# Kernel tuning notes

Measured on AMD Instinct MI355X. Metric: run time of the kernel, lower is better.

Reference implementation:

```python
import jax, jax.numpy as jnp
import numpy as np

N, E, C, H, EDGE_DIM, HID = 50000, 800000, 128, 8, 64, 512
D = C // H  # head dim = out_channels_conv


def layer_norm(x, g, b, eps=1e-5):
    mu = x.mean(-1, keepdims=True)
    var = ((x - mu) ** 2).mean(-1, keepdims=True)
    return (x - mu) * jax.lax.rsqrt(var + eps) * g + b


def _lin_init(k, fan_in, fan_out):
    s = 1.0 / np.sqrt(fan_in)
    kw, kb = jax.random.split(k)
    w = jax.random.uniform(kw, (fan_in, fan_out), minval=-s, maxval=s, dtype=jnp.float32)
    b = jax.random.uniform(kb, (fan_out,), minval=-s, maxval=s, dtype=jnp.float32)
    return w, b


def setup_inputs() -> dict:
    key = jax.random.key(0)
    ks = jax.random.split(key, 16)
    wq, bq = _lin_init(ks[0], C, C)
    wk, bk = _lin_init(ks[1], C, C)
    wv, bv = _lin_init(ks[2], C, C)
    ws, bs = _lin_init(ks[3], C, C)          # lin_self
    we, be = _lin_init(ks[4], EDGE_DIM, C)   # lin_edge
    wp, bp = _lin_init(ks[5], C, C)          # projection
    w1, b1 = _lin_init(ks[6], C, HID)        # node_dst_mlp[0]
    w2, b2 = _lin_init(ks[7], HID, C)        # node_dst_mlp[2]
    x = jax.random.normal(ks[8], (N, C), dtype=jnp.float32)
    edge_attr = jax.random.normal(ks[9], (E, EDGE_DIM), dtype=jnp.float32)
    edge_index = jax.random.randint(ks[10], (2, E), 0, N, dtype=jnp.int64)
    return dict(
        x=x, edge_attr=edge_attr, edge_index=edge_index,
        wq=wq, bq=bq, wk=wk, bk=bk, wv=wv, bv=bv, ws=ws, bs=bs,
        we=we, be=be, wp=wp, bp=bp, w1=w1, b1=b1, w2=w2, b2=b2,
        ln1_g=jnp.ones((C,), jnp.float32), ln1_b=jnp.zeros((C,), jnp.float32),
        ln2_g=jnp.ones((C,), jnp.float32), ln2_b=jnp.zeros((C,), jnp.float32),
    )


def reference(x, edge_attr, edge_index,
              wq, bq, wk, bk, wv, bv, ws, bs, we, be, wp, bp,
              w1, b1, w2, b2, ln1_g, ln1_b, ln2_g, ln2_b):
    src, dst = edge_index[0], edge_index[1]

    x_skip = x
    xn = layer_norm(x, ln1_g, ln1_b)                       # layer_norm_attention
    x_r = xn @ ws + bs                                     # lin_self residual
    q = (xn @ wq + bq).reshape(N, H, D)
    k = (xn @ wk + bk).reshape(N, H, D)
    v = (xn @ wv + bv).reshape(N, H, D)
    e = (edge_attr @ we + be).reshape(E, H, D)             # lin_edge (edge_pre_mlp = Identity)

    # edge-indexed multi-head attention: softmax over incoming edges per dst node
    ke = k[src] + e                                        # [E,H,D]
    alpha = jnp.einsum('ehd,ehd->eh', q[dst], ke) / np.sqrt(D)   # [E,H]
    amax = jax.lax.stop_gradient(jax.ops.segment_max(alpha, dst, num_segments=N))
    ex = jnp.exp(alpha - amax[dst])
    den = jax.ops.segment_sum(ex, dst, num_segments=N)
    w = ex / (den[dst] + 1e-16)                            # [E,H]
    out = jax.ops.segment_sum(w[:, :, None] * (v[src] + e), dst, num_segments=N)  # [N,H,D]
    out = out.reshape(N, C)

    out = (out + x_r) @ wp + bp                            # projection
    out = out + x_skip
    h = layer_norm(out, ln2_g, ln2_b)                      # layer_norm_mlp_dst
    h = jax.nn.gelu(h @ w1 + b1) @ w2 + b2                 # node_dst_mlp
    nodes_new = out + h
    return nodes_new, edge_attr
```

## Files before the change

kernel.cpp:

```cpp
#include <hip/hip_runtime.h>
#include <hip/hip_bf16.h>
#include <cstdio>

#define NN 50000
#define NE 800000
#define CC 128
#define EDIM 64
#define HIDN 512

using bf16 = __hip_bfloat16;
typedef short sh8 __attribute__((ext_vector_type(8)));
typedef float f32x4 __attribute__((ext_vector_type(4)));

static __device__ __forceinline__ float b2f(bf16 v){ return __bfloat162float(v); }
static __device__ __forceinline__ bf16 f2b(float v){ return __float2bfloat16(v); }
static __device__ __forceinline__ float u2f(unsigned short u){
    union { unsigned int i; float f; } w; w.i = ((unsigned int)u) << 16; return w.f;
}
static __device__ __forceinline__ unsigned short f2u(float f){
    bf16 b = __float2bfloat16(f);
    return *reinterpret_cast<unsigned short*>(&b);
}
static __device__ __forceinline__ float2 loadbf2(const bf16* p){
    __hip_bfloat162 v = *reinterpret_cast<const __hip_bfloat162*>(p);
    return make_float2(__bfloat162float(v.x), __bfloat162float(v.y));
}
static __device__ __forceinline__ float gelu_tanh(float x){
    const float c = 0.7978845608028654f;
    float u = c * (x + 0.044715f * x * x * x);
    return x / (1.0f + __expf(-2.0f * u));
}

constexpr size_t AL(size_t x){ return (x + 255) & ~(size_t)255; }
constexpr size_t OFF_FLAG = 0;
constexpr size_t OFF_DEG  = 256;
constexpr size_t OFF_ROW  = AL(OFF_DEG + (size_t)(NN + 1) * 4);
constexpr size_t OFF_CUR  = AL(OFF_ROW + (size_t)(NN + 1) * 4);
constexpr size_t OFF_EPOS = AL(OFF_CUR + (size_t)NN * 4);
constexpr size_t OFF_SRC  = AL(OFF_EPOS + (size_t)NE * 4);
constexpr size_t OFF_DST  = AL(OFF_SRC + (size_t)NE * 4);
constexpr size_t OFF_QC   = AL(OFF_DST + (size_t)NE * 4);
constexpr size_t OFF_KC   = AL(OFF_QC  + (size_t)NN * CC * 2);
constexpr size_t OFF_VC   = AL(OFF_KC  + (size_t)NN * CC * 2);
constexpr size_t OFF_ATT  = AL(OFF_VC  + (size_t)NN * CC * 2);
constexpr size_t OFF_PRM  = AL(OFF_ATT + (size_t)NN * CC * 2);
constexpr size_t PRM_ELEMS = 4*(16384+128) + 8192+128 + 16384+128 + 65536+512 + 65536+128 + 4*128;
constexpr size_t OFF_ALP  = AL(OFF_PRM + PRM_ELEMS * 2);
constexpr size_t OFF_VP   = AL(OFF_ALP + (size_t)NE * 8 * 4);
constexpr size_t OFF_XRC  = AL(OFF_VP + (size_t)NE * CC * 2);
constexpr size_t OFF_WFQ  = AL(OFF_XRC + (size_t)NN * CC * 2);
constexpr size_t OFF_WFK  = OFF_WFQ + 32768;
constexpr size_t OFF_WFV  = OFF_WFK + 32768;
constexpr size_t OFF_WFS  = OFF_WFV + 32768;
constexpr size_t OFF_WFP  = OFF_WFS + 32768;
constexpr size_t OFF_WF1  = OFF_WFP + 32768;
constexpr size_t OFF_WF2  = OFF_WF1 + 131072;
constexpr size_t OFF_WFE  = OFF_WF2 + 131072;
constexpr size_t OFF_BSUM = OFF_WFE + 16384;
constexpr size_t WS_NEED  = OFF_BSUM + 256;

__global__ void k_detect(const unsigned short* xw, const unsigned int* ew, int* flags){
    __shared__ int sw, sz;
    if (threadIdx.x == 0){ sw = 0; sz = 0; }
    __syncthreads();
    int w = 0;
    for (int i = threadIdx.x; i < 8192; i += 256){
        unsigned e = (xw[i] >> 7) & 0xFF;
        if (e == 0xFF || (e != 0 && (e < 0x60 || e > 0x90))) w++;
    }
    atomicAdd(&sw, w);
    int z = 0;
    for (int i = threadIdx.x; i < 2048; i += 256)
        if (ew[2*i+1] == 0u) z++;
    atomicAdd(&sz, z);
    __syncthreads();
    if (threadIdx.x == 0){
        flags[0] = (sw > 2048) ? 1 : 0;
        flags[1] = (sz > 1536) ? 1 : 0;
    }
}

struct CvtJob { const void* s; bf16* d; int n; };
struct CvtJobs { CvtJob j[20]; };
__global__ void k_cvt_all(CvtJobs jobs, const int* flags){
    const int f = flags[0];
    const int e = blockIdx.x >> 5;
    const CvtJob J = jobs.j[e];
    const int stride = 32 * 256;
    for (int i = (blockIdx.x & 31) * 256 + threadIdx.x; i < J.n; i += stride){
        if (f) J.d[i] = f2b(((const float*)J.s)[i]);
        else   J.d[i] = ((const bf16*)J.s)[i];
    }
}

__global__ void k_cvt_idx(const int* e32, int* srcI, int* dstI, int* deg, const int* flags){
    const int f = flags[1];
    int i = blockIdx.x * blockDim.x + threadIdx.x;
    const int stride = gridDim.x * blockDim.x;
    if (f){
        const long long* e64 = (const long long*)e32;
        for (; i < NE; i += stride){
            srcI[i] = (int)e64[i];
            const int d = (int)e64[NE + i];
            dstI[i] = d;
            atomicAdd(&deg[d], 1);
        }
    } else {
        for (; i < NE; i += stride){
            srcI[i] = e32[i];
            const int d = e32[NE + i];
            dstI[i] = d;
            atomicAdd(&deg[d], 1);
        }
    }
}

struct WJob { const bf16* W; bf16* WF; int K; int N; };
struct WJobs { WJob j[8]; };
__global__ void k_wprep_all(WJobs jobs){
    const WJob J = jobs.j[blockIdx.x / 48];
    const int KS = J.K >> 5;
    const int total = J.K * J.N;
    for (int o = (blockIdx.x % 48) * 256 + threadIdx.x; o < total; o += 48 * 256){
        const int j  = o & 7;
        const int ln = (o >> 3) & 63;
        const int tt = o >> 9;
        const int ks = tt % KS, ct = tt / KS;
        const int kk = (ks << 5) + ((ln >> 4) << 3) + j;
        const int c  = (ct << 4) + (ln & 15);
        J.WF[o] = J.W[kk * J.N + c];
    }
}

#define ASWZ(row, chunk)  (((row) << 8)  + ((((chunk) ^ ((row) & 15))) << 4))
#define HSWZ(row, chunk)  (((row) << 10) + ((((chunk) ^ ((row) & 15))) << 4))
#define EASWZ(row, chunk) (((row) << 7)  + ((((chunk) ^ ((row) & 7)))  << 4))

static __device__ __forceinline__ void gemm_nodes_128(
    const unsigned short* Abase, int row0, int lane,
    const bf16* __restrict__ WF, const bf16* __restrict__ bias,
    bf16* __restrict__ outp, int n0)
{
    const int rA = row0 + (lane & 15);
    sh8 af[4];
    #pragma unroll
    for (int ks = 0; ks < 4; ++ks)
        af[ks] = *(const sh8*)((const char*)Abase + ASWZ(rA, (ks << 2) + (lane >> 4)));
    f32x4 acc[8] = {};
    #pragma unroll
    for (int ks = 0; ks < 4; ++ks)
        #pragma unroll
        for (int ct = 0; ct < 8; ++ct){
            sh8 bfr = *(const sh8*)(WF + ((size_t)((ct << 2) + ks) * 64 + lane) * 8);
            acc[ct] = __builtin_amdgcn_mfma_f32_16x16x32_bf16(af[ks], bfr, acc[ct], 0, 0, 0);
        }
    #pragma unroll
    for (int ct = 0; ct < 8; ++ct){
        const int c = (ct << 4) + (lane & 15);
        const float bv = b2f(bias[c]);
        #pragma unroll
        for (int i = 0; i < 4; ++i){
            const int r = row0 + ((lane >> 4) << 2) + i;
            if (n0 + r < NN)
                outp[(size_t)(n0 + r) * CC + c] = f2b(acc[ct][i] + bv);
        }
    }
}

__global__ __launch_bounds__(256) void k_node_pre2(
    const void* __restrict__ x_raw, const int* __restrict__ flags,
    const bf16* __restrict__ WFq, const bf16* __restrict__ bq,
    const bf16* __restrict__ WFk, const bf16* __restrict__ bk,
    const bf16* __restrict__ WFv, const bf16* __restrict__ bv,
    const bf16* __restrict__ WFs, const bf16* __restrict__ bs,
    const bf16* __restrict__ g,  const bf16* __restrict__ bb,
    bf16* __restrict__ q, bf16* __restrict__ k, bf16* __restrict__ v,
    bf16* __restrict__ xr)
{
    __shared__ unsigned short A[64 * 128];
    const int t = threadIdx.x, lane = t & 63, wid = t >> 6;
    const int n0 = blockIdx.x * 64;

    if (flags[0]){
        const float* x = (const float*)x_raw;
        #pragma unroll
        for (int it = 0; it < 8; ++it){
            const int u = t + 256 * it;
            const int row = u >> 5, c = (u & 31) << 2;
            float4 a = make_float4(0.f, 0.f, 0.f, 0.f);
            if (n0 + row < NN)
                a = *(const float4*)&x[(size_t)(n0 + row) * CC + c];
            ushort4 b;
            b.x = f2u(a.x); b.y = f2u(a.y); b.z = f2u(a.z); b.w = f2u(a.w);
            *(ushort4*)((char*)A + ASWZ(row, c >> 3) + ((c & 7) << 1)) = b;
        }
    } else {
        const bf16* x = (const bf16*)x_raw;
        #pragma unroll
        for (int it = 0; it < 4; ++it){
            const int c8 = t + 256 * it;
            const int row = c8 >> 4, chunk = c8 & 15, col = chunk << 3;
            uint4 val = make_uint4(0u, 0u, 0u, 0u);
            if (n0 + row < NN)
                val = *(const uint4*)&x[(size_t)(n0 + row) * CC + col];
            *(uint4*)((char*)A + ASWZ(row, chunk)) = val;
        }
    }
    __syncthreads();

    {
        const int nd = wid * 16 + (lane & 15), qd = lane >> 4;
        float vals[32];
        #pragma unroll
        for (int i = 0; i < 4; ++i){
            uint4 u = *(const uint4*)((const char*)A + ASWZ(nd, (qd << 2) + i));
            unsigned uu[4] = {u.x, u.y, u.z, u.w};
            #pragma unroll
            for (int j2 = 0; j2 < 4; ++j2){
                vals[i*8 + j2*2]     = u2f((unsigned short)(uu[j2] & 0xFFFF));
                vals[i*8 + j2*2 + 1] = u2f((unsigned short)(uu[j2] >> 16));
            }
        }
        float s = 0.f;
        #pragma unroll
        for (int i = 0; i < 32; ++i) s += vals[i];
        s += __shfl_xor(s, 16); s += __shfl_xor(s, 32);
        const float mu = s * (1.0f / CC);
        float vv = 0.f;
        #pragma unroll
        for (int i = 0; i < 32; ++i){ const float d = vals[i] - mu; vv += d * d; }
        vv += __shfl_xor(vv, 16); vv += __shfl_xor(vv, 32);
        const float rstd = rsqrtf(vv * (1.0f / CC) + 1e-5f);
        #pragma unroll
        for (int i = 0; i < 4; ++i){
            unsigned w[4];
            #pragma unroll
            for (int j2 = 0; j2 < 4; ++j2){
                const int c0 = qd * 32 + i * 8 + j2 * 2;
                const float a0 = (vals[i*8+j2*2]   - mu) * rstd * b2f(g[c0])   + b2f(bb[c0]);
                const float a1 = (vals[i*8+j2*2+1] - mu) * rstd * b2f(g[c0+1]) + b2f(bb[c0+1]);
                w[j2] = (unsigned)f2u(a0) | ((unsigned)f2u(a1) << 16);
            }
            *(uint4*)((char*)A + ASWZ(nd, (qd << 2) + i)) = make_uint4(w[0], w[1], w[2], w[3]);
        }
    }
    __syncthreads();

    const int row0 = wid * 16;
    gemm_nodes_128(A, row0, lane, WFq, bq, q,  n0);
    gemm_nodes_128(A, row0, lane, WFk, bk, k,  n0);
    gemm_nodes_128(A, row0, lane, WFv, bv, v,  n0);
    gemm_nodes_128(A, row0, lane, WFs, bs, xr, n0);
}

__global__ __launch_bounds__(1024) void k_scan1(const int* __restrict__ deg,
                                                int* __restrict__ row, int* __restrict__ bsum){
    __shared__ int sb[1024];
    const int t = threadIdx.x;
    const int idx = blockIdx.x * 1024 + t;
    sb[t] = (idx < NN) ? deg[idx] : 0;
    __syncthreads();
    for (int off = 1; off < 1024; off <<= 1){
        int tv = (t >= off) ? sb[t - off] : 0;
        __syncthreads();
        sb[t] += tv;
        __syncthreads();
    }
    if (idx < NN) row[idx + 1] = sb[t];
    if (t == 1023) bsum[blockIdx.x] = sb[1023];
}

__global__ void k_scan2(int* __restrict__ bsum, int nb){
    int v = (threadIdx.x < nb) ? bsum[threadIdx.x] : 0;
    for (int off = 1; off < 64; off <<= 1){
        int u = __shfl_up(v, off);
        if (threadIdx.x >= off) v += u;
    }
    if (threadIdx.x < nb) bsum[threadIdx.x] = v;
}

__global__ __launch_bounds__(1024) void k_scan3(const int* __restrict__ bsum, int* __restrict__ row){
    const int idx = blockIdx.x * 1024 + threadIdx.x;
    const int add = (blockIdx.x > 0) ? bsum[blockIdx.x - 1] : 0;
    if (idx < NN) row[idx + 1] += add;
    if (idx == 0) row[0] = 0;
}

__global__ void k_scatter(const int* __restrict__ dst, const int* __restrict__ rowstart,
                          int* __restrict__ cursor, int* __restrict__ epos){
    const int i = blockIdx.x * blockDim.x + threadIdx.x;
    if (i < NE) {
        const int d = dst[i];
        const int p = atomicAdd(&cursor[d], 1);
        epos[i] = rowstart[d] + p;
    }
}

__global__ __launch_bounds__(256) void k_edge3(
    const void* __restrict__ ea_raw, const int* __restrict__ flags,
    const bf16* __restrict__ WFe, const bf16* __restrict__ be,
    const bf16* __restrict__ kv_q, const bf16* __restrict__ kv_k, const bf16* __restrict__ kv_v,
    const int* __restrict__ srcI, const int* __restrict__ dstI, const int* __restrict__ epos,
    float* __restrict__ alphap, unsigned short* __restrict__ vperm)
{
    __shared__ unsigned short EA[64 * 64];
    __shared__ unsigned short ET[64 * 128];
    const int t = threadIdx.x, lane = t & 63, wid = t >> 6;
    const int e0 = blockIdx.x * 64;

    if (flags[0]){
        const float* ea = (const float*)ea_raw;
        #pragma unroll
        for (int it = 0; it < 4; ++it){
            const int u = t + 256 * it;
            const int row = u >> 4, c = (u & 15) << 2;
            const float4 a = *(const float4*)&ea[(size_t)(e0 + row) * EDIM + c];
            ushort4 b;
            b.x = f2u(a.x); b.y = f2u(a.y); b.z = f2u(a.z); b.w = f2u(a.w);
            *(ushort4*)((char*)EA + EASWZ(row, c >> 3) + ((c & 7) << 1)) = b;
        }
    } else {
        const unsigned short* ea = (const unsigned short*)ea_raw;
        #pragma unroll
        for (int it = 0; it < 2; ++it){
            const int u = t + 256 * it;
            const int row = u >> 3, c = (u & 7) << 3;
            ushort4 lo = *(const ushort4*)&ea[(size_t)(e0 + row) * EDIM + c];
            ushort4 hi = *(const ushort4*)&ea[(size_t)(e0 + row) * EDIM + c + 4];
            *(ushort4*)((char*)EA + EASWZ(row, c >> 3)) = lo;
            *(ushort4*)((char*)EA + EASWZ(row, c >> 3) + 8) = hi;
        }
    }
    __syncthreads();

    const int row0 = wid * 16;
    {
        const int rA = row0 + (lane & 15);
        sh8 af[2];
        #pragma unroll
        for (int ks = 0; ks < 2; ++ks)
            af[ks] = *(const sh8*)((const char*)EA + EASWZ(rA, (ks << 2) + (lane >> 4)));
        f32x4 acc[8] = {};
        #pragma unroll
        for (int ks = 0; ks < 2; ++ks)
            #pragma unroll
            for (int ct = 0; ct < 8; ++ct){
                sh8 bfr = *(const sh8*)(WFe + ((size_t)((ct << 1) + ks) * 64 + lane) * 8);
                acc[ct] = __builtin_amdgcn_mfma_f32_16x16x32_bf16(af[ks], bfr, acc[ct], 0, 0, 0);
            }
        #pragma unroll
        for (int ct = 0; ct < 8; ++ct){
            const int c = (ct << 4) + (lane & 15);
            const float bv = b2f(be[c]);
            #pragma unroll
            for (int i = 0; i < 4; ++i){
                const int r = row0 + ((lane >> 4) << 2) + i;
                *(unsigned short*)((char*)ET + ASWZ(r, c >> 3) + ((c & 7) << 1)) =
                    f2u(acc[ct][i] + bv);
            }
        }
    }
    __syncthreads();

    const int g = t >> 5, cT = t & 31, c = cT << 2;
    #pragma unroll
    for (int i = 0; i < 8; ++i){
        const int eid = e0 + g * 8 + i;
        const int s = srcI[eid];
        const int d = dstI[eid];
        const int p = epos[eid];
        const ushort4 ev = *(const ushort4*)((const char*)ET + ASWZ(g * 8 + i, c >> 3) + ((c & 7) << 1));
        const ushort4 kr = *(const ushort4*)&kv_k[(size_t)s * CC + c];
        const ushort4 vr = *(const ushort4*)&kv_v[(size_t)s * CC + c];
        const ushort4 qr = *(const ushort4*)&kv_q[(size_t)d * CC + c];
        const float e0_ = u2f(ev.x), e1_ = u2f(ev.y), e2_ = u2f(ev.z), e3_ = u2f(ev.w);
        float part = u2f(qr.x) * (e0_ + u2f(kr.x)) + u2f(qr.y) * (e1_ + u2f(kr.y))
                   + u2f(qr.z) * (e2_ + u2f(kr.z)) + u2f(qr.w) * (e3_ + u2f(kr.w));
        part += __shfl_xor(part, 1);
        part += __shfl_xor(part, 2);
        if ((cT & 3) == 0)
            alphap[(size_t)p * 8 + (cT >> 2)] = part * 0.25f;
        ushort4 vo;
        vo.x = f2u(e0_ + u2f(vr.x)); vo.y = f2u(e1_ + u2f(vr.y));
        vo.z = f2u(e2_ + u2f(vr.z)); vo.w = f2u(e3_ + u2f(vr.w));
        *(ushort4*)&vperm[(size_t)p * CC + c] = vo;
    }
}

__global__ __launch_bounds__(256) void k_attn3(
    const float* __restrict__ alphap, const bf16* __restrict__ vperm,
    const int* __restrict__ rowstart, bf16* __restrict__ attn_bf)
{
    const int t = threadIdx.x, lane = t & 63, wid = t >> 6;
    const int n = blockIdx.x * 4 + wid;
    const int h = lane >> 3;

    float m = -INFINITY, den = 0.0f;
    float2 num = make_float2(0.0f, 0.0f);

    const int jb = rowstart[n], je = rowstart[n + 1];
    for (int j = jb; j < je; ++j) {
        const float alpha = alphap[(size_t)j * 8 + h];
        const float2 v2 = loadbf2(&vperm[(size_t)j * CC + 2 * lane]);
        if (alpha > m) {
            const float sc = __expf(m - alpha);
            den *= sc; num.x *= sc; num.y *= sc;
            m = alpha;
        }
        const float p = __expf(alpha - m);
        den += p;
        num.x += p * v2.x;
        num.y += p * v2.y;
    }
    const float inv = 1.0f / (den + 1e-16f);
    __hip_bfloat162 pr;
    pr.x = f2b(num.x * inv);
    pr.y = f2b(num.y * inv);
    *reinterpret_cast<__hip_bfloat162*>(&attn_bf[(size_t)n * CC + 2 * lane]) = pr;
}

__global__ __launch_bounds__(256) void k_post2(
    const bf16* __restrict__ attn_bf, const bf16* __restrict__ xr,
    const void* __restrict__ x_raw,
    const bf16* __restrict__ WFp, const bf16* __restrict__ bp,
    const bf16* __restrict__ WF1, const bf16* __restrict__ b1,
    const bf16* __restrict__ WF2, const bf16* __restrict__ b2c,
    const bf16* __restrict__ g2, const bf16* __restrict__ bb2,
    void* __restrict__ outv, const int* __restrict__ flags)
{
    __shared__ unsigned short A[64 * 128];
    __shared__ unsigned short HID[64 * 512];
    const int t = threadIdx.x, lane = t & 63, wid = t >> 6;
    const int n0 = blockIdx.x * 64;
    const int f32io = flags[0];

    #pragma unroll
    for (int it = 0; it < 4; ++it){
        const int c8 = t + 256 * it;
        const int row = c8 >> 4, chunk = c8 & 15, col = chunk << 3;
        unsigned w[4] = {0u, 0u, 0u, 0u};
        if (n0 + row < NN){
            const size_t o = (size_t)(n0 + row) * CC + col;
            uint4 a4 = *(const uint4*)&attn_bf[o];
            uint4 r4 = *(const uint4*)&xr[o];
            unsigned au[4] = {a4.x, a4.y, a4.z, a4.w};
            unsigned ru[4] = {r4.x, r4.y, r4.z, r4.w};
            #pragma unroll
            for (int j2 = 0; j2 < 4; ++j2){
                const float lo = u2f((unsigned short)(au[j2] & 0xFFFF)) +
                                 u2f((unsigned short)(ru[j2] & 0xFFFF));
                const float hi = u2f((unsigned short)(au[j2] >> 16)) +
                                 u2f((unsigned short)(ru[j2] >> 16));
                w[j2] = (unsigned)f2u(lo) | ((unsigned)f2u(hi) << 16);
            }
        }
        *(uint4*)((char*)A + ASWZ(row, chunk)) = make_uint4(w[0], w[1], w[2], w[3]);
    }
    __syncthreads();

    const int row0 = wid * 16;
    const int rA = row0 + (lane & 15);

    float out2[8][4];
    {
        sh8 af[4];
        #pragma unroll
        for (int ks = 0; ks < 4; ++ks)
            af[ks] = *(const sh8*)((const char*)A + ASWZ(rA, (ks << 2) + (lane >> 4)));
        f32x4 acc[8] = {};
        #pragma unroll
        for (int ks = 0; ks < 4; ++ks)
            #pragma unroll
            for (int ct = 0; ct < 8; ++ct){
                sh8 bfr = *(const sh8*)(WFp + ((size_t)((ct << 2) + ks) * 64 + lane) * 8);
                acc[ct] = __builtin_amdgcn_mfma_f32_16x16x32_bf16(af[ks], bfr, acc[ct], 0, 0, 0);
            }
        #pragma unroll
        for (int ct = 0; ct < 8; ++ct){
            const int c = (ct << 4) + (lane & 15);
            const float bv = b2f(bp[c]);
            #pragma unroll
            for (int i = 0; i < 4; ++i){
                const int r = row0 + ((lane >> 4) << 2) + i;
                float xs = 0.f;
                if (n0 + r < NN){
                    const size_t o = (size_t)(n0 + r) * CC + c;
                    xs = f32io ? ((const float*)x_raw)[o] : b2f(((const bf16*)x_raw)[o]);
                }
                out2[ct][i] = acc[ct][i] + bv + xs;
            }
        }
    }

    {
        float mu[4], rstd[4];
        #pragma unroll
        for (int i = 0; i < 4; ++i){
            float s = 0.f;
            #pragma unroll
            for (int ct = 0; ct < 8; ++ct) s += out2[ct][i];
            s += __shfl_xor(s, 1); s += __shfl_xor(s, 2);
            s += __shfl_xor(s, 4); s += __shfl_xor(s, 8);
            mu[i] = s * (1.0f / CC);
        }
        #pragma unroll
        for (int i = 0; i < 4; ++i){
            float vv = 0.f;
            #pragma unroll
            for (int ct = 0; ct < 8; ++ct){ const float d = out2[ct][i] - mu[i]; vv += d * d; }
            vv += __shfl_xor(vv, 1); vv += __shfl_xor(vv, 2);
            vv += __shfl_xor(vv, 4); vv += __shfl_xor(vv, 8);
            rstd[i] = rsqrtf(vv * (1.0f / CC) + 1e-5f);
        }
        #pragma unroll
        for (int ct = 0; ct < 8; ++ct){
            const int c = (ct << 4) + (lane & 15);
            const float gv = b2f(g2[c]), bbv = b2f(bb2[c]);
            const int chunk = c >> 3;
            #pragma unroll
            for (int i = 0; i < 4; ++i){
                const int r = row0 + ((lane >> 4) << 2) + i;
                const float ln = (out2[ct][i] - mu[i]) * rstd[i] * gv + bbv;
                *(unsigned short*)((char*)A + ASWZ(r, chunk) + ((c & 7) << 1)) = f2u(ln);
            }
        }
    }

    {
        sh8 af[4];
        #pragma unroll
        for (int ks = 0; ks < 4; ++ks)
            af[ks] = *(const sh8*)((const char*)A + ASWZ(rA, (ks << 2) + (lane >> 4)));
        #pragma unroll
        for (int grp = 0; grp < 4; ++grp){
            f32x4 acc[8] = {};
            #pragma unroll
            for (int ks = 0; ks < 4; ++ks)
                #pragma unroll
                for (int ctl = 0; ctl < 8; ++ctl){
                    const int ct = grp * 8 + ctl;
                    sh8 bfr = *(const sh8*)(WF1 + ((size_t)((ct << 2) + ks) * 64 + lane) * 8);
                    acc[ctl] = __builtin_amdgcn_mfma_f32_16x16x32_bf16(af[ks], bfr, acc[ctl], 0, 0, 0);
                }
            #pragma unroll
            for (int ctl = 0; ctl < 8; ++ctl){
                const int ct = grp * 8 + ctl;
                const int c = (ct << 4) + (lane & 15);
                const float bv = b2f(b1[c]);
                const int chunk = c >> 3;
                #pragma unroll
                for (int i = 0; i < 4; ++i){
                    const int r = row0 + ((lane >> 4) << 2) + i;
                    const float h = gelu_tanh(acc[ctl][i] + bv);
                    *(unsigned short*)((char*)HID + HSWZ(r, chunk) + ((c & 7) << 1)) = f2u(h);
                }
            }
        }
    }

    {
        f32x4 acc[8] = {};
        #pragma unroll
        for (int ks = 0; ks < 16; ++ks){
            sh8 afh = *(const sh8*)((const char*)HID + HSWZ(rA, (ks << 2) + (lane >> 4)));
            #pragma unroll
            for (int ct = 0; ct < 8; ++ct){
                sh8 bfr = *(const sh8*)(WF2 + ((size_t)((ct << 4) + ks) * 64 + lane) * 8);
                acc[ct] = __builtin_amdgcn_mfma_f32_16x16x32_bf16(afh, bfr, acc[ct], 0, 0, 0);
            }
        }
        #pragma unroll
        for (int ct = 0; ct < 8; ++ct){
            const int c = (ct << 4) + (lane & 15);
            const float bv = b2f(b2c[c]);
            #pragma unroll
            for (int i = 0; i < 4; ++i){
                const int r = row0 + ((lane >> 4) << 2) + i;
                if (n0 + r < NN){
                    const float val = out2[ct][i] + acc[ct][i] + bv;
                    if (f32io) ((float*)outv)[(size_t)(n0 + r) * CC + c] = val;
                    else       ((bf16*)outv)[(size_t)(n0 + r) * CC + c] = f2b(val);
                }
            }
        }
    }
}

__global__ void k_edgecopy(const void* __restrict__ ea, void* __restrict__ outv,
                           const int* __restrict__ flags){
    size_t i = (size_t)blockIdx.x * blockDim.x + threadIdx.x;
    const size_t stride = (size_t)gridDim.x * blockDim.x;
    if (flags[0]) {
        const uint4* s = (const uint4*)ea;
        uint4* d = (uint4*)((float*)outv + (size_t)NN * CC);
        const size_t n4 = (size_t)NE * EDIM / 4;
        for (; i < n4; i += stride) d[i] = s[i];
    } else {
        const uint4* s = (const uint4*)ea;
        uint4* d = (uint4*)((bf16*)outv + (size_t)NN * CC);
        const size_t n4 = (size_t)NE * EDIM / 8;
        for (; i < n4; i += stride) d[i] = s[i];
    }
}

extern "C" void kernel_launch(void* const* d_in, const int* in_sizes, int n_in,
                              void* d_out, int out_size, void* d_ws, size_t ws_size,
                              hipStream_t stream)
{
    if (ws_size < WS_NEED) {
        fprintf(stderr, "[kl] WS TOO SMALL ws=%zu need=%zu\n", ws_size, WS_NEED);
        return;
    }

    char* ws = (char*)d_ws;
    int*  flags = (int*)(ws + OFF_FLAG);
    int*  deg   = (int*)(ws + OFF_DEG);
    int*  row   = (int*)(ws + OFF_ROW);
    int*  cur   = (int*)(ws + OFF_CUR);
    int*  epos  = (int*)(ws + OFF_EPOS);
    int*  srcI  = (int*)(ws + OFF_SRC);
    int*  dstI  = (int*)(ws + OFF_DST);
    int*  bsum  = (int*)(ws + OFF_BSUM);
    bf16* qC    = (bf16*)(ws + OFF_QC);
    bf16* kC    = (bf16*)(ws + OFF_KC);
    bf16* vC    = (bf16*)(ws + OFF_VC);
    bf16* attC  = (bf16*)(ws + OFF_ATT);
    bf16* xrC   = (bf16*)(ws + OFF_XRC);
    float* alphap = (float*)(ws + OFF_ALP);
    unsigned short* vperm = (unsigned short*)(ws + OFF_VP);
    bf16* WFq = (bf16*)(ws + OFF_WFQ);
    bf16* WFk = (bf16*)(ws + OFF_WFK);
    bf16* WFv = (bf16*)(ws + OFF_WFV);
    bf16* WFs = (bf16*)(ws + OFF_WFS);
    bf16* WFp = (bf16*)(ws + OFF_WFP);
    bf16* WF1 = (bf16*)(ws + OFF_WF1);
    bf16* WF2 = (bf16*)(ws + OFF_WF2);
    bf16* WFe = (bf16*)(ws + OFF_WFE);

    bf16* P = (bf16*)(ws + OFF_PRM);
    bf16 *wqC=P; P+=16384; bf16 *bqC=P; P+=128;
    bf16 *wkC=P; P+=16384; bf16 *bkC=P; P+=128;
    bf16 *wvC=P; P+=16384; bf16 *bvC=P; P+=128;
    bf16 *wsC=P; P+=16384; bf16 *bsC=P; P+=128;
    bf16 *weC=P; P+=8192;  bf16 *beC=P; P+=128;
    bf16 *wpC=P; P+=16384; bf16 *bpC=P; P+=128;
    bf16 *w1C=P; P+=65536; bf16 *b1C=P; P+=512;
    bf16 *w2C=P; P+=65536; bf16 *b2C=P; P+=128;
    bf16 *g1C=P; P+=128;   bf16 *n1C=P; P+=128;
    bf16 *g2C=P; P+=128;   bf16 *n2C=P; P+=128;

    hipMemsetAsync(deg, 0, (size_t)(NN + 1) * sizeof(int), stream);
    hipMemsetAsync(cur, 0, (size_t)NN * sizeof(int), stream);

    k_detect<<<1, 256, 0, stream>>>((const unsigned short*)d_in[0],
                                    (const unsigned int*)d_in[2], flags);

    {
        CvtJobs cj;
        bf16* dsts[20] = {wqC,bqC,wkC,bkC,wvC,bvC,wsC,bsC,weC,beC,
                          wpC,bpC,w1C,b1C,w2C,b2C,g1C,n1C,g2C,n2C};
        const int ns[20] = {16384,128,16384,128,16384,128,16384,128,8192,128,
                            16384,128,65536,512,65536,128,128,128,128,128};
        for (int i = 0; i < 20; ++i){ cj.j[i].s = d_in[3 + i]; cj.j[i].d = dsts[i]; cj.j[i].n = ns[i]; }
        k_cvt_all<<<20 * 32, 256, 0, stream>>>(cj, flags);
    }
    k_cvt_idx<<<1024, 256, 0, stream>>>((const int*)d_in[2], srcI, dstI, deg, flags);

    {
        WJobs wj;
        const WJob js[8] = {{wqC,WFq,128,128},{wkC,WFk,128,128},{wvC,WFv,128,128},
                            {wsC,WFs,128,128},{wpC,WFp,128,128},{w1C,WF1,128,512},
                            {w2C,WF2,512,128},{weC,WFe,64,128}};
        for (int i = 0; i < 8; ++i) wj.j[i] = js[i];
        k_wprep_all<<<8 * 48, 256, 0, stream>>>(wj);
    }

    const int NB64 = (NN + 63) / 64;
    const int NSC  = (NN + 1023) / 1024;
    k_node_pre2<<<NB64, 256, 0, stream>>>(d_in[0], flags, WFq, bqC, WFk, bkC, WFv, bvC,
                                          WFs, bsC, g1C, n1C, qC, kC, vC, xrC);
    k_scan1<<<NSC, 1024, 0, stream>>>(deg, row, bsum);
    k_scan2<<<1, 64, 0, stream>>>(bsum, NSC);
    k_scan3<<<NSC, 1024, 0, stream>>>(bsum, row);
    k_scatter<<<(NE + 255) / 256, 256, 0, stream>>>(dstI, row, cur, epos);
    k_edge3<<<NE / 64, 256, 0, stream>>>(d_in[1], flags, WFe, beC, qC, kC, vC,
                                         srcI, dstI, epos, alphap, vperm);
    k_attn3<<<NN / 4, 256, 0, stream>>>(alphap, (const bf16*)vperm, row, attC);
    k_post2<<<NB64, 256, 0, stream>>>(attC, xrC, d_in[0], WFp, bpC, WF1, b1C, WF2, b2C,
                                      g2C, n2C, d_out, flags);
    k_edgecopy<<<2048, 256, 0, stream>>>(d_in[1], d_out, flags);
}
```

Baseline: 595.7 us.

## Fuse edge_attr output copy into edge kernel and batch gather loads

The separate edge-attribute copy kernel is removed. The edge kernel now writes edge_attr to the output while it already has the tile loaded for the edge projection, which avoids a second full read of the large edge tensor and one kernel launch. The per-edge index, k, v and q gathers are also hoisted into arrays so that all eight edges' loads are issued before the compute, increasing memory-level parallelism. This raises register pressure and may reduce occupancy.

```diff
diff --git a/kernel.cpp b/kernel.cpp
--- a/kernel.cpp
+++ b/kernel.cpp
@@ -296,12 +296,13 @@
     }
 }
 
-__global__ __launch_bounds__(256) void k_edge3(
+__global__ __launch_bounds__(256) void k_edge4(
     const void* __restrict__ ea_raw, const int* __restrict__ flags,
     const bf16* __restrict__ WFe, const bf16* __restrict__ be,
     const bf16* __restrict__ kv_q, const bf16* __restrict__ kv_k, const bf16* __restrict__ kv_v,
     const int* __restrict__ srcI, const int* __restrict__ dstI, const int* __restrict__ epos,
-    float* __restrict__ alphap, unsigned short* __restrict__ vperm)
+    float* __restrict__ alphap, unsigned short* __restrict__ vperm,
+    void* __restrict__ outv)
 {
     __shared__ unsigned short EA[64 * 64];
     __shared__ unsigned short ET[64 * 128];
@@ -310,25 +311,29 @@
 
     if (flags[0]){
         const float* ea = (const float*)ea_raw;
+        float* outd = (float*)outv + (size_t)NN * CC;
         #pragma unroll
         for (int it = 0; it < 4; ++it){
             const int u = t + 256 * it;
             const int row = u >> 4, c = (u & 15) << 2;
-            const float4 a = *(const float4*)&ea[(size_t)(e0 + row) * EDIM + c];
+            const size_t o = (size_t)(e0 + row) * EDIM + c;
+            const float4 a = *(const float4*)&ea[o];
+            *(float4*)&outd[o] = a;
             ushort4 b;
             b.x = f2u(a.x); b.y = f2u(a.y); b.z = f2u(a.z); b.w = f2u(a.w);
             *(ushort4*)((char*)EA + EASWZ(row, c >> 3) + ((c & 7) << 1)) = b;
         }
     } else {
         const unsigned short* ea = (const unsigned short*)ea_raw;
+        unsigned short* outd = (unsigned short*)outv + (size_t)NN * CC;
         #pragma unroll
         for (int it = 0; it < 2; ++it){
             const int u = t + 256 * it;
             const int row = u >> 3, c = (u & 7) << 3;
-            ushort4 lo = *(const ushort4*)&ea[(size_t)(e0 + row) * EDIM + c];
-            ushort4 hi = *(const ushort4*)&ea[(size_t)(e0 + row) * EDIM + c + 4];
-            *(ushort4*)((char*)EA + EASWZ(row, c >> 3)) = lo;
-            *(ushort4*)((char*)EA + EASWZ(row, c >> 3) + 8) = hi;
+            const size_t o = (size_t)(e0 + row) * EDIM + c;
+            uint4 raw = *(const uint4*)&ea[o];
+            *(uint4*)&outd[o] = raw;
+            *(uint4*)((char*)EA + EASWZ(row, c >> 3)) = raw;
         }
     }
     __syncthreads();
@@ -363,27 +368,35 @@
     __syncthreads();
 
     const int g = t >> 5, cT = t & 31, c = cT << 2;
+    int s8[8], d8[8], p8[8];
     #pragma unroll
     for (int i = 0; i < 8; ++i){
         const int eid = e0 + g * 8 + i;
-        const int s = srcI[eid];
-        const int d = dstI[eid];
-        const int p = epos[eid];
+        s8[i] = srcI[eid];
+        d8[i] = dstI[eid];
+        p8[i] = epos[eid];
+    }
+    ushort4 kr[8], vr[8], qr[8];
+    #pragma unroll
+    for (int i = 0; i < 8; ++i) kr[i] = *(const ushort4*)&kv_k[(size_t)s8[i] * CC + c];
+    #pragma unroll
+    for (int i = 0; i < 8; ++i) vr[i] = *(const ushort4*)&kv_v[(size_t)s8[i] * CC + c];
+    #pragma unroll
+    for (int i = 0; i < 8; ++i) qr[i] = *(const ushort4*)&kv_q[(size_t)d8[i] * CC + c];
+    #pragma unroll
+    for (int i = 0; i < 8; ++i){
         const ushort4 ev = *(const ushort4*)((const char*)ET + ASWZ(g * 8 + i, c >> 3) + ((c & 7) << 1));
-        const ushort4 kr = *(const ushort4*)&kv_k[(size_t)s * CC + c];
-        const ushort4 vr = *(const ushort4*)&kv_v[(size_t)s * CC + c];
-        const ushort4 qr = *(const ushort4*)&kv_q[(size_t)d * CC + c];
         const float e0_ = u2f(ev.x), e1_ = u2f(ev.y), e2_ = u2f(ev.z), e3_ = u2f(ev.w);
-        float part = u2f(qr.x) * (e0_ + u2f(kr.x)) + u2f(qr.y) * (e1_ + u2f(kr.y))
-                   + u2f(qr.z) * (e2_ + u2f(kr.z)) + u2f(qr.w) * (e3_ + u2f(kr.w));
+        float part = u2f(qr[i].x) * (e0_ + u2f(kr[i].x)) + u2f(qr[i].y) * (e1_ + u2f(kr[i].y))
+                   + u2f(qr[i].z) * (e2_ + u2f(kr[i].z)) + u2f(qr[i].w) * (e3_ + u2f(kr[i].w));
         part += __shfl_xor(part, 1);
         part += __shfl_xor(part, 2);
         if ((cT & 3) == 0)
-            alphap[(size_t)p * 8 + (cT >> 2)] = part * 0.25f;
+            alphap[(size_t)p8[i] * 8 + (cT >> 2)] = part * 0.25f;
         ushort4 vo;
-        vo.x = f2u(e0_ + u2f(vr.x)); vo.y = f2u(e1_ + u2f(vr.y));
-        vo.z = f2u(e2_ + u2f(vr.z)); vo.w = f2u(e3_ + u2f(vr.w));
-        *(ushort4*)&vperm[(size_t)p * CC + c] = vo;
+        vo.x = f2u(e0_ + u2f(vr[i].x)); vo.y = f2u(e1_ + u2f(vr[i].y));
+        vo.z = f2u(e2_ + u2f(vr[i].z)); vo.w = f2u(e3_ + u2f(vr[i].w));
+        *(ushort4*)&vperm[(size_t)p8[i] * CC + c] = vo;
     }
 }
 
@@ -583,23 +596,6 @@
                 }
             }
         }
-    }
-}
-
-__global__ void k_edgecopy(const void* __restrict__ ea, void* __restrict__ outv,
-                           const int* __restrict__ flags){
-    size_t i = (size_t)blockIdx.x * blockDim.x + threadIdx.x;
-    const size_t stride = (size_t)gridDim.x * blockDim.x;
-    if (flags[0]) {
-        const uint4* s = (const uint4*)ea;
-        uint4* d = (uint4*)((float*)outv + (size_t)NN * CC);
-        const size_t n4 = (size_t)NE * EDIM / 4;
-        for (; i < n4; i += stride) d[i] = s[i];
-    } else {
-        const uint4* s = (const uint4*)ea;
-        uint4* d = (uint4*)((bf16*)outv + (size_t)NN * CC);
-        const size_t n4 = (size_t)NE * EDIM / 8;
-        for (; i < n4; i += stride) d[i] = s[i];
     }
 }
 
@@ -683,10 +679,9 @@
     k_scan2<<<1, 64, 0, stream>>>(bsum, NSC);
     k_scan3<<<NSC, 1024, 0, stream>>>(bsum, row);
     k_scatter<<<(NE + 255) / 256, 256, 0, stream>>>(dstI, row, cur, epos);
-    k_edge3<<<NE / 64, 256, 0, stream>>>(d_in[1], flags, WFe, beC, qC, kC, vC,
-                                         srcI, dstI, epos, alphap, vperm);
+    k_edge4<<<NE / 64, 256, 0, stream>>>(d_in[1], flags, WFe, beC, qC, kC, vC,
+                                         srcI, dstI, epos, alphap, vperm, d_out);
     k_attn3<<<NN / 4, 256, 0, stream>>>(alphap, (const bf16*)vperm, row, attC);
     k_post2<<<NB64, 256, 0, stream>>>(attC, xrC, d_in[0], WFp, bpC, WF1, b1C, WF2, b2C,
                                       g2C, n2C, d_out, flags);
-    k_edgecopy<<<2048, 256, 0, stream>>>(d_in[1], d_out, flags);
-}
+}
```

After: 537.4 us. -9.8%, faster.
